# Kernel tuning notes

Hardware: AMD Instinct MI355X
Metric: run time of the kernel (lower is better)

Reference implementation:

```python
import jax, jax.numpy as jnp
import numpy as np

# Dims: B batch, T target seq, S source seq (self-attn: S==T), V symmetry-rep dim (D4 -> 8),
# M heads-per-group, K groups (num_heads = M*K = 8), F head_rep dim (TrivialRep -> 1),
# Hqk qk head width, Hv v head width, C feature width per rep component.
B, T, S, V, M, K, F, Hqk, Hv, C = 4, 512, 512, 8, 2, 4, 1, 32, 32, 256


def setup_inputs() -> dict:
    key = jax.random.key(0)
    ks = jax.random.split(key, 6)
    x = jax.random.normal(ks[0], (B, T, V, C), jnp.float32)
    # SymDecompLinear kernels: q has extra out reps (F, M, K); k/v have (F, 1, K) -> m axis broadcast
    Wq = jax.random.normal(ks[1], (C, M, K, F, Hqk), jnp.float32) / np.sqrt(C).astype(np.float32)
    Wk = jax.random.normal(ks[2], (C, K, F, Hqk), jnp.float32) / np.sqrt(C).astype(np.float32)
    Wv = jax.random.normal(ks[3], (C, K, F, Hv), jnp.float32) / np.sqrt(C).astype(np.float32)
    # out projection contracts the (M, K, F, Hv) head structure back to C features
    Wout = jax.random.normal(ks[4], (M, K, F, Hv, C), jnp.float32) / np.sqrt(M * K * F * Hv).astype(np.float32)
    mask = jax.random.bernoulli(ks[5], 0.9, (B, T, S))
    mask = mask.at[..., 0].set(True)  # guarantee each query attends to >=1 key
    return dict(x=x, Wq=Wq, Wk=Wk, Wv=Wv, Wout=Wout, mask=mask)


def reference(x, Wq, Wk, Wv, Wout, mask):
    # projections: q -> [B,T,V,M,K,F,Hqk]; k,v -> [B,S,V,K,F,H] (single head per group, broadcast over m)
    q = jnp.einsum('btvc,cmkfh->btvmkfh', x, Wq)
    k = jnp.einsum('bsvc,ckfh->bsvkfh', x, Wk)
    v = jnp.einsum('bsvc,ckfh->bsvkfh', x, Wv)
    scale = 1.0 / np.sqrt(F * Hqk).astype(np.float32)
    # logits retain the symmetry axis v: [B,T,S,V,M,K]
    logits = scale * jnp.einsum('btvmkfh,bsvkfh->btsvmk', q, k)
    lgmsk = mask[..., :, :, None, None, None]  # [B,T,S,1,1,1]
    weight = jax.nn.softmax(logits, axis=-4, where=lgmsk)  # softmax over source axis s
    att = jnp.einsum('btsvmk,bsvkfh->btvmkfh', weight, v)
    out = jnp.einsum('btvmkfh,mkfhc->btvc', att, Wout)
    return out
```

## Files before the change

### kernel.cpp

```cpp
#include <hip/hip_runtime.h>
#include <hip/hip_bf16.h>
#include <cstdint>

#define BB 4
#define TT 512
#define SS 512
#define VV 8
#define NROWS (BB * TT * VV)


typedef __attribute__((ext_vector_type(8))) short bf16x8;
typedef __attribute__((ext_vector_type(4))) float f32x4;

static __device__ __forceinline__ short f2bf(float f) {
  union { float f; unsigned u; } x; x.f = f;
  unsigned r = x.u + 0x7FFFu + ((x.u >> 16) & 1u);
  return (short)(r >> 16);
}

static __device__ __forceinline__ unsigned cvt_pk(float lo, float hi) {
  unsigned r;
  asm("v_cvt_pk_bf16_f32 %0, %1, %2" : "=v"(r) : "v"(lo), "v"(hi));
  return r;
}

__global__ __launch_bounds__(256) void pack_all_kernel(const float* __restrict__ Wq,
                                                       const float* __restrict__ Wk,
                                                       const float* __restrict__ Wv,
                                                       const float* __restrict__ Wout,
                                                       const int* __restrict__ mask,
                                                       short* __restrict__ WcatT,
                                                       short* __restrict__ WoutT,
                                                       unsigned long long* __restrict__ mask64) {
  if (blockIdx.x < 768) {
    int idx = blockIdx.x * 256 + threadIdx.x;
    const float qscale = 0.17677669529663687f * 1.4426950408889634f;
    if (idx < 512 * 256) {
      int n = idx >> 8, c = idx & 255;
      float val;
      if (n < 256)      val = Wq[c * 256 + n] * qscale;
      else if (n < 384) val = Wk[c * 128 + (n - 256)];
      else              val = Wv[c * 128 + (n - 384)];
      WcatT[idx] = f2bf(val);
    } else {
      int j = idx - 512 * 256;
      int cc = j >> 8, jj = j & 255;
      WoutT[j] = f2bf(Wout[jj * 256 + cc]);
    }
  } else {
    int row = (blockIdx.x - 768) * 4 + (threadIdx.x >> 6);
    int ln = threadIdx.x & 63;
    const int* mrow = mask + (size_t)row * SS;
#pragma unroll
    for (int c = 0; c < 8; ++c) {
      unsigned long long bal = __ballot(mrow[c * 64 + ln] != 0);
      if (ln == 0) mask64[(size_t)row * 8 + c] = bal;
    }
  }
}

__global__ __launch_bounds__(256) void vtrans_kernel(const short* __restrict__ qkvh,
                                                     short* __restrict__ Vt2) {
  const int hd = blockIdx.x;
  const int bv = hd >> 2, k = hd & 3;
  const int s0 = threadIdx.x * 2;
  const short* src = qkvh + ((size_t)(bv * 16 + 12 + k) * 512 + s0) * 32;
  bf16x8 r0[4], r1[4];
#pragma unroll
  for (int i = 0; i < 4; ++i) {
    r0[i] = *(const bf16x8*)(src + i * 8);
    r1[i] = *(const bf16x8*)(src + 32 + i * 8);
  }
  short* dst = Vt2 + (size_t)hd * 16384 + (s0 >> 6) * 2048 + (s0 & 63);
#pragma unroll
  for (int h = 0; h < 32; ++h) {
    unsigned pk = (unsigned)(unsigned short)r0[h >> 3][h & 7] |
                  ((unsigned)(unsigned short)r1[h >> 3][h & 7] << 16);
    *(unsigned*)(dst + h * 64) = pk;
  }
}

template <int N, bool AF32, int EPI>
__global__ __launch_bounds__(256) void gemm_bf16(const void* __restrict__ Ap,
                                                 const short* __restrict__ Bt,
                                                 void* __restrict__ Cout) {
  __shared__ short As[128][64];
  __shared__ short Bs[128][64];
  const int tid = threadIdx.x;
  const int w = tid >> 6, ln = tid & 63;
  const int wr = (w >> 1) * 64, wc = (w & 1) * 64;
  const int bm = blockIdx.x * 128, bn = blockIdx.y * 128;
  const int lr = ln & 15, lk = (ln >> 4) * 8;
  const int r0 = tid >> 3, ko = (tid & 7) * 8;

  f32x4 acc[4][4] = {};

  for (int k0 = 0; k0 < 256; k0 += 64) {
    bf16x8 a[4], bb[4];
#pragma unroll
    for (int i = 0; i < 4; ++i) {
      size_t row = (size_t)(bm + i * 32 + r0);
      if constexpr (AF32) {
        const float* Af = (const float*)Ap;
        float4 f0 = *(const float4*)&Af[row * 256 + k0 + ko];
        float4 f1 = *(const float4*)&Af[row * 256 + k0 + ko + 4];
        uint4 pk = make_uint4(cvt_pk(f0.x, f0.y), cvt_pk(f0.z, f0.w),
                              cvt_pk(f1.x, f1.y), cvt_pk(f1.z, f1.w));
        a[i] = *(bf16x8*)&pk;
      } else {
        a[i] = *(const bf16x8*)&((const short*)Ap)[row * 256 + k0 + ko];
      }
      bb[i] = *(const bf16x8*)&Bt[(size_t)(bn + i * 32 + r0) * 256 + k0 + ko];
    }
    __syncthreads();
#pragma unroll
    for (int i = 0; i < 4; ++i) {
      *(bf16x8*)&As[i * 32 + r0][ko] = a[i];
      *(bf16x8*)&Bs[i * 32 + r0][ko] = bb[i];
    }
    __syncthreads();

#pragma unroll
    for (int kk = 0; kk < 2; ++kk) {
      bf16x8 af[4], bfr[4];
#pragma unroll
      for (int mi = 0; mi < 4; ++mi)
        af[mi] = *(const bf16x8*)&As[wr + mi * 16 + lr][kk * 32 + lk];
#pragma unroll
      for (int ni = 0; ni < 4; ++ni)
        bfr[ni] = *(const bf16x8*)&Bs[wc + ni * 16 + lr][kk * 32 + lk];
#pragma unroll
      for (int mi = 0; mi < 4; ++mi)
#pragma unroll
        for (int ni = 0; ni < 4; ++ni)
          acc[mi][ni] = __builtin_amdgcn_mfma_f32_16x16x32_bf16(af[mi], bfr[ni], acc[mi][ni], 0, 0, 0);
    }
  }

  const int rowg = (ln >> 4) * 4;
  if constexpr (EPI == 0) {
#pragma unroll
    for (int mi = 0; mi < 4; ++mi)
#pragma unroll
      for (int r = 0; r < 4; ++r) {
        size_t row = bm + wr + mi * 16 + rowg + r;
#pragma unroll
        for (int ni = 0; ni < 4; ++ni)
          ((float*)Cout)[row * N + bn + wc + ni * 16 + lr] = acc[mi][ni][r];
      }
  } else {
    int soff[4];
#pragma unroll
    for (int ni = 0; ni < 4; ++ni) {
      int j = bn + wc + ni * 16 + lr;
      soff[ni] = (j >> 5) * (512 * 32) + (j & 31);
    }
    short* q16 = (short*)Cout;
#pragma unroll
    for (int mi = 0; mi < 4; ++mi)
#pragma unroll
      for (int r = 0; r < 4; ++r) {
        int row = bm + wr + mi * 16 + rowg + r;
        int t = (row >> 3) & 511;
        int bv = (row >> 12) * 8 + (row & 7);
        size_t base = ((size_t)bv << 18) + (t << 5);
        unsigned u0 = cvt_pk(acc[mi][0][r], acc[mi][1][r]);
        unsigned u1 = cvt_pk(acc[mi][2][r], acc[mi][3][r]);
        q16[base + soff[0]] = (short)u0;
        q16[base + soff[1]] = (short)(u0 >> 16);
        q16[base + soff[2]] = (short)u1;
        q16[base + soff[3]] = (short)(u1 >> 16);
      }
  }
}

__global__ __launch_bounds__(256) void attn_mfma(const short* __restrict__ qkvh,
                                                 const short* __restrict__ Vt2,
                                                 const unsigned long long* __restrict__ mask64,
                                                 short* __restrict__ att) {
  const int t0 = blockIdx.x * 64;
  const int v  = blockIdx.y >> 2;
  const int k  = blockIdx.y & 3;
  const int b  = blockIdx.z;
  const int tid = threadIdx.x;
  const int w  = tid >> 6;
  const int ln = tid & 63;
  const int gq = ln >> 4;
  const int tr = ln & 15;
  const int bv = b * 8 + v;

  __shared__ __align__(16) short Pt[4][16][72];

  bf16x8 qf[2];
  {
    const short* qp = qkvh + ((size_t)(bv * 16 + k) * 512 + (t0 + w * 16 + tr)) * 32 + gq * 8;
    qf[0] = *(const bf16x8*)qp;
    qf[1] = *(const bf16x8*)(qp + 4 * 512 * 32);
  }

  f32x4 acc_o[2][2] = {};
  float l_run[2] = {0.f, 0.f};

  const short* kb = qkvh + (size_t)(bv * 16 + 8 + k) * 16384 + gq * 8;
  const short* vb = Vt2 + (size_t)(bv * 4 + k) * 16384 + tr * 64 + gq * 8;
  const unsigned long long* mrow = mask64 + ((size_t)(b * TT + t0 + w * 16 + tr)) * 8;

  bf16x8 kf[4], vf[2][2];
  unsigned long long mb;
#pragma unroll
  for (int st = 0; st < 4; ++st)
    kf[st] = *(const bf16x8*)(kb + (size_t)(st * 16 + tr) * 32);
#pragma unroll
  for (int sh = 0; sh < 2; ++sh)
#pragma unroll
    for (int hh = 0; hh < 2; ++hh)
      vf[sh][hh] = *(const bf16x8*)(vb + hh * 16 * 64 + sh * 32);
  mb = mrow[0];

  for (int c = 0; c < 8; ++c) {
    bf16x8 kn[4], vn[2][2];
    unsigned long long mbn;
    if (c < 7) {
#pragma unroll
      for (int st = 0; st < 4; ++st)
        kn[st] = *(const bf16x8*)(kb + (size_t)((c + 1) * 64 + st * 16 + tr) * 32);
#pragma unroll
      for (int sh = 0; sh < 2; ++sh)
#pragma unroll
        for (int hh = 0; hh < 2; ++hh)
          vn[sh][hh] = *(const bf16x8*)(vb + (c + 1) * 2048 + hh * 16 * 64 + sh * 32);
      mbn = mrow[c + 1];
    }

    unsigned mlo = (unsigned)mb, mhi = (unsigned)(mb >> 32);
    float bias[4][4];
#pragma unroll
    for (int st = 0; st < 4; ++st) {
      unsigned wbits = (st < 2) ? mlo : mhi;
      const int base = (st & 1) * 16 + 4 * gq;
#pragma unroll
      for (int r = 0; r < 4; ++r)
        bias[st][r] = ((wbits >> (base + r)) & 1u) ? 0.f : -INFINITY;
    }

#pragma unroll
    for (int m = 0; m < 2; ++m) {
      f32x4 lac[4];
#pragma unroll
      for (int st = 0; st < 4; ++st) {
        f32x4 z = {0.f, 0.f, 0.f, 0.f};
        lac[st] = __builtin_amdgcn_mfma_f32_16x16x32_bf16(kf[st], qf[m], z, 0, 0, 0);
      }
      float pl[4][4];
      float rs = 0.f;
#pragma unroll
      for (int st = 0; st < 4; ++st)
#pragma unroll
        for (int r = 0; r < 4; ++r) {
          pl[st][r] = exp2f(lac[st][r] + bias[st][r]);
          rs += pl[st][r];
        }
      rs += __shfl_xor(rs, 16);
      rs += __shfl_xor(rs, 32);
      l_run[m] += rs;

#pragma unroll
      for (int st = 0; st < 4; ++st)
        *(uint2*)&Pt[w][tr][st * 16 + 4 * gq] =
            make_uint2(cvt_pk(pl[st][0], pl[st][1]), cvt_pk(pl[st][2], pl[st][3]));
#pragma unroll
      for (int sh = 0; sh < 2; ++sh) {
        bf16x8 pf = *(const bf16x8*)&Pt[w][tr][sh * 32 + gq * 8];
#pragma unroll
        for (int hh = 0; hh < 2; ++hh)
          acc_o[m][hh] = __builtin_amdgcn_mfma_f32_16x16x32_bf16(pf, vf[sh][hh], acc_o[m][hh], 0, 0, 0);
      }
    }

    if (c < 7) {
#pragma unroll
      for (int st = 0; st < 4; ++st) kf[st] = kn[st];
#pragma unroll
      for (int sh = 0; sh < 2; ++sh)
#pragma unroll
        for (int hh = 0; hh < 2; ++hh) vf[sh][hh] = vn[sh][hh];
      mb = mbn;
    }
  }

#pragma unroll
  for (int m = 0; m < 2; ++m) {
    float invR[4];
#pragma unroll
    for (int r = 0; r < 4; ++r) invR[r] = 1.f / __shfl(l_run[m], 4 * gq + r);
#pragma unroll
    for (int r = 0; r < 4; ++r) {
      short* dst = att + ((size_t)((b * TT + t0 + w * 16 + 4 * gq + r) * VV + v)) * 256
                 + m * 128 + k * 32 + tr;
      unsigned u = cvt_pk(acc_o[m][0][r] * invR[r], acc_o[m][1][r] * invR[r]);
      dst[0]  = (short)u;
      dst[16] = (short)(u >> 16);
    }
  }
}

extern "C" void kernel_launch(void* const* d_in, const int* in_sizes, int n_in,
                              void* d_out, int out_size, void* d_ws, size_t ws_size,
                              hipStream_t stream) {
  const float* x = (const float*)d_in[0];
  const float* Wq = (const float*)d_in[1];
  const float* Wk = (const float*)d_in[2];
  const float* Wv = (const float*)d_in[3];
  const float* Wout = (const float*)d_in[4];
  const int* mask = (const int*)d_in[5];
  float* out = (float*)d_out;

  short* WcatT = (short*)d_ws;
  short* WoutT = WcatT + 512 * 256;
  short* qkvh  = WoutT + 256 * 256;
  short* att   = qkvh + (size_t)NROWS * 512;
  short* Vt2   = att + (size_t)NROWS * 256;
  unsigned long long* mask64 = (unsigned long long*)(Vt2 + (size_t)128 * 16384);

  pack_all_kernel<<<768 + 512, 256, 0, stream>>>(Wq, Wk, Wv, Wout, mask, WcatT, WoutT, mask64);
  gemm_bf16<512, true, 2><<<dim3(NROWS / 128, 4), 256, 0, stream>>>(x, WcatT, qkvh);
  vtrans_kernel<<<128, 256, 0, stream>>>(qkvh, Vt2);
  attn_mfma<<<dim3(TT / 64, VV * 4, BB), 256, 0, stream>>>(qkvh, Vt2, mask64, att);
  gemm_bf16<256, false, 0><<<dim3(NROWS / 128, 2), 256, 0, stream>>>(att, WoutT, out);
}
```

Baseline: 68.55 us.

## Fuse V transpose into QKV GEMM epilogue and remap attention grid

New measurement: 69.35 us. Within noise of the previous version (+1.2%).

```diff
diff --git a/kernel.cpp b/kernel.cpp
--- a/kernel.cpp
+++ b/kernel.cpp
@@ -59,31 +59,11 @@
   }
 }
 
-__global__ __launch_bounds__(256) void vtrans_kernel(const short* __restrict__ qkvh,
-                                                     short* __restrict__ Vt2) {
-  const int hd = blockIdx.x;
-  const int bv = hd >> 2, k = hd & 3;
-  const int s0 = threadIdx.x * 2;
-  const short* src = qkvh + ((size_t)(bv * 16 + 12 + k) * 512 + s0) * 32;
-  bf16x8 r0[4], r1[4];
-#pragma unroll
-  for (int i = 0; i < 4; ++i) {
-    r0[i] = *(const bf16x8*)(src + i * 8);
-    r1[i] = *(const bf16x8*)(src + 32 + i * 8);
-  }
-  short* dst = Vt2 + (size_t)hd * 16384 + (s0 >> 6) * 2048 + (s0 & 63);
-#pragma unroll
-  for (int h = 0; h < 32; ++h) {
-    unsigned pk = (unsigned)(unsigned short)r0[h >> 3][h & 7] |
-                  ((unsigned)(unsigned short)r1[h >> 3][h & 7] << 16);
-    *(unsigned*)(dst + h * 64) = pk;
-  }
-}
-
 template <int N, bool AF32, int EPI>
 __global__ __launch_bounds__(256) void gemm_bf16(const void* __restrict__ Ap,
                                                  const short* __restrict__ Bt,
-                                                 void* __restrict__ Cout) {
+                                                 void* __restrict__ Cout,
+                                                 short* __restrict__ Vt2) {
   __shared__ short As[128][64];
   __shared__ short Bs[128][64];
   const int tid = threadIdx.x;
@@ -149,11 +129,12 @@
           ((float*)Cout)[row * N + bn + wc + ni * 16 + lr] = acc[mi][ni][r];
       }
   } else {
-    int soff[4];
+    int slotN[4], h16[4];
 #pragma unroll
     for (int ni = 0; ni < 4; ++ni) {
-      int j = bn + wc + ni * 16 + lr;
-      soff[ni] = (j >> 5) * (512 * 32) + (j & 31);
+      int jb = bn + wc + ni * 16;
+      slotN[ni] = jb >> 5;
+      h16[ni] = jb & 16;
     }
     short* q16 = (short*)Cout;
 #pragma unroll
@@ -163,13 +144,18 @@
         int row = bm + wr + mi * 16 + rowg + r;
         int t = (row >> 3) & 511;
         int bv = (row >> 12) * 8 + (row & 7);
-        size_t base = ((size_t)bv << 18) + (t << 5);
         unsigned u0 = cvt_pk(acc[mi][0][r], acc[mi][1][r]);
         unsigned u1 = cvt_pk(acc[mi][2][r], acc[mi][3][r]);
-        q16[base + soff[0]] = (short)u0;
-        q16[base + soff[1]] = (short)(u0 >> 16);
-        q16[base + soff[2]] = (short)u1;
-        q16[base + soff[3]] = (short)(u1 >> 16);
+        short vals[4] = {(short)u0, (short)(u0 >> 16), (short)u1, (short)(u1 >> 16)};
+#pragma unroll
+        for (int ni = 0; ni < 4; ++ni) {
+          int slot = slotN[ni], h = h16[ni] + lr;
+          if (slot < 12) {
+            q16[((size_t)bv << 18) + slot * 16384 + t * 32 + h] = vals[ni];
+          } else {
+            Vt2[(((size_t)bv * 4 + (slot - 12)) << 14) + ((t >> 6) << 11) + (h << 6) + (t & 63)] = vals[ni];
+          }
+        }
       }
   }
 }
@@ -178,16 +164,19 @@
                                                  const short* __restrict__ Vt2,
                                                  const unsigned long long* __restrict__ mask64,
                                                  short* __restrict__ att) {
-  const int t0 = blockIdx.x * 64;
-  const int v  = blockIdx.y >> 2;
-  const int k  = blockIdx.y & 3;
-  const int b  = blockIdx.z;
+  const int orig = blockIdx.x;
+  const int widx = (orig & 7) * 128 + (orig >> 3);
+  const int head = widx >> 3;
+  const int t0 = (widx & 7) * 64;
+  const int bv = head >> 2;
+  const int b  = bv >> 3;
+  const int v  = bv & 7;
+  const int k  = head & 3;
   const int tid = threadIdx.x;
   const int w  = tid >> 6;
   const int ln = tid & 63;
   const int gq = ln >> 4;
   const int tr = ln & 15;
-  const int bv = b * 8 + v;
 
   __shared__ __align__(16) short Pt[4][16][72];
 
@@ -323,8 +312,7 @@
   unsigned long long* mask64 = (unsigned long long*)(Vt2 + (size_t)128 * 16384);
 
   pack_all_kernel<<<768 + 512, 256, 0, stream>>>(Wq, Wk, Wv, Wout, mask, WcatT, WoutT, mask64);
-  gemm_bf16<512, true, 2><<<dim3(NROWS / 128, 4), 256, 0, stream>>>(x, WcatT, qkvh);
-  vtrans_kernel<<<128, 256, 0, stream>>>(qkvh, Vt2);
-  attn_mfma<<<dim3(TT / 64, VV * 4, BB), 256, 0, stream>>>(qkvh, Vt2, mask64, att);
-  gemm_bf16<256, false, 0><<<dim3(NROWS / 128, 2), 256, 0, stream>>>(att, WoutT, out);
-}
+  gemm_bf16<512, true, 2><<<dim3(NROWS / 128, 4), 256, 0, stream>>>(x, WcatT, qkvh, Vt2);
+  attn_mfma<<<1024, 256, 0, stream>>>(qkvh, Vt2, mask64, att);
+  gemm_bf16<256, false, 0><<<dim3(NROWS / 128, 2), 256, 0, stream>>>(att, WoutT, out, nullptr);
+}
```
